# Kernel optimization log

Measured on AMD Instinct MI355X. Metric: run time of the kernel, lower is better.

## Reference

```python
import jax, jax.numpy as jnp
import numpy as np

N_PTILES = 4096
MAX_SOURCES = 1
PTILE_SLEN = 53  # odd -> slen == ptile_slen, size_lens is identity
N_BANDS = 1


def setup_inputs() -> dict:
    key = jax.random.key(0)
    k1, k2, k3, k4, k5, k6 = jax.random.split(key, 6)
    shape = (N_PTILES, MAX_SOURCES)
    gal = jax.random.uniform(k1, shape + (7,), dtype=jnp.float32)
    # realistic SIE lens params per _sample_lens_params: b in [5,30], q in (0,1)
    b = jax.random.uniform(k2, shape + (1,), dtype=jnp.float32) * 25.0 + 5.0
    centers = jax.random.normal(k3, shape + (2,), dtype=jnp.float32)
    q = jax.random.uniform(k4, shape + (1,), dtype=jnp.float32) * 0.8 + 0.1
    beta = (jax.random.uniform(k5, shape + (1,), dtype=jnp.float32) - 0.5) * (np.pi / 2)
    ellf = (1.0 - q) / (1.0 + q)
    e1 = ellf * jnp.cos(beta)
    e2 = ellf * jnp.sin(beta)
    lens_params = jnp.concatenate([gal, b, centers, e1, e2], axis=-1)  # [..., 12]
    bools = (jax.random.uniform(k6, shape + (1,), dtype=jnp.float32) < 0.7).astype(jnp.float32)
    return {"lens_params": lens_params, "lensed_galaxy_bools": bools}


def _render_unlensed(gal_p, slen):
    # Differentiable Gaussian stand-in for the (CPU galsim) unlensed source render.
    c = jnp.arange(slen, dtype=jnp.float32) - (slen - 1) / 2.0
    yy, xx = jnp.meshgrid(c, c, indexing="ij")
    flux = gal_p[:, 0] * 1000.0 + 100.0      # [N]
    sigma = gal_p[:, 3] * 3.0 + 1.0          # [N]
    r2 = xx[None] ** 2 + yy[None] ** 2       # [1, S, S]
    s2 = (sigma ** 2)[:, None, None]
    return flux[:, None, None] * jnp.exp(-0.5 * r2 / s2) / (2.0 * np.pi * s2)


def _sie_deflection(x, y, lens_p):
    # x, y: [1, S, S]; lens_p: [N, 5] -> (xg, yg): [N, S, S]
    b, cx, cy, e1, e2 = [lens_p[:, i][:, None, None] for i in range(5)]
    ell = jnp.sqrt(e1 ** 2 + e2 ** 2)
    q = (1.0 - ell) / (1.0 + ell)
    phirad = jnp.arctan(e2 / e1)
    cosp, sinp = jnp.cos(phirad), jnp.sin(phirad)
    xsie = (x - cx) * cosp + (y - cy) * sinp
    ysie = (y - cy) * cosp - (x - cx) * sinp
    r_ell = jnp.sqrt(q * xsie ** 2 + ysie ** 2 / q + 1e-12)
    qfact = jnp.sqrt(1.0 / q - q)
    eps = 0.001
    safe = jnp.maximum(qfact, eps)
    denom = r_ell + (r_ell == 0)
    xtg = jnp.where(qfact >= eps, b / safe * jnp.arctan(safe * xsie / denom), b * xsie / denom)
    ytg = jnp.where(qfact >= eps, b / safe * jnp.arctanh(safe * ysie / denom), b * ysie / denom)
    xg = xtg * cosp - ytg * sinp
    yg = ytg * cosp + xtg * sinp
    return xg, yg


def _bilinear(im, xs, ys):
    # im: [N, S, S]; xs (col coord), ys (row coord): [N, S, S]
    N, S, _ = im.shape
    x0 = jnp.clip(jnp.floor(xs).astype(jnp.int32), 0, S - 1)
    x1 = jnp.clip(jnp.floor(xs).astype(jnp.int32) + 1, 0, S - 1)
    y0 = jnp.clip(jnp.floor(ys).astype(jnp.int32), 0, S - 1)
    y1 = jnp.clip(jnp.floor(ys).astype(jnp.int32) + 1, 0, S - 1)
    flat = im.reshape(N, S * S)

    def g(yi, xi):
        return jnp.take_along_axis(flat, (yi * S + xi).reshape(N, -1), axis=1).reshape(N, S, S)

    x0f, x1f = x0.astype(im.dtype), x1.astype(im.dtype)
    y0f, y1f = y0.astype(im.dtype), y1.astype(im.dtype)
    # weights use the CLIPPED integer corners, matching bilinear_interpolate_numpy
    wa = (x1f - xs) * (y1f - ys)
    wb = (x1f - xs) * (ys - y0f)
    wc = (xs - x0f) * (y1f - ys)
    wd = (xs - x0f) * (ys - y0f)
    return g(y0, x0) * wa + g(y1, x0) * wb + g(y0, x1) * wc + g(y1, x1) * wd


def _forward(lens_params, lensed_galaxy_bools):
    n_ptiles, max_s, P = lens_params.shape
    z = lens_params.reshape(-1, P)
    gal_p, lens_p = z[:, :7], z[:, 7:]
    slen = PTILE_SLEN
    unlensed = _render_unlensed(gal_p, slen)            # [N, S, S]
    # grid exactly as lens_galsim: range [-nx//2, nx//2] over nx points
    nx = slen
    lo = float((-nx) // 2)   # -27 for nx=53
    hi = float(nx // 2)      # 26
    coords = (hi - lo) * jnp.arange(nx, dtype=jnp.float32) / (nx - 1) + lo
    x = jnp.broadcast_to(coords[None, :], (nx, nx))  # varies along columns
    y = jnp.broadcast_to(coords[:, None], (nx, nx))  # varies along rows
    xg, yg = _sie_deflection(x[None], y[None], lens_p)
    shift = float(nx // 2)
    lensed = _bilinear(unlensed, x[None] - xg + shift, y[None] - yg + shift)
    out = lensed.reshape(n_ptiles, max_s, N_BANDS, slen, slen)
    # render-all + mask is equivalent to the zeros-init + boolean-fill + final mask
    return out * lensed_galaxy_bools[..., None, None]


def reference(lens_params, lensed_galaxy_bools):
    return _forward(lens_params, lensed_galaxy_bools)
```

## Files before the change

kernel.cpp:

```cpp
#include <hip/hip_runtime.h>
#include <math.h>

#define SLEN 53
#define NPIX 2809
#define NPARAM 12
#define BLK 256
#define PW 16
#define NSLOT 11

__device__ __forceinline__ float fast_atan(float u) {
    float t = __builtin_fabsf(u);
    float rin = __builtin_amdgcn_rcpf(t);
    bool big = t > 1.0f;
    float w = big ? rin : t;
    bool mid = w > 0.4142135624f;
    float w2 = (w - 1.0f) * __builtin_amdgcn_rcpf(w + 1.0f);
    float x = mid ? w2 : w;
    float z = x * x;
    float p = ((8.05374449538e-2f * z - 1.38776856032e-1f) * z
               + 1.99777106478e-1f) * z - 3.33329491539e-1f;
    float r = __builtin_fmaf(p * z, x, x);
    r = mid ? r + 0.78539816339744831f : r;
    r = big ? 1.57079632679489662f - r : r;
    return __builtin_copysignf(r, u);
}

__device__ __forceinline__ float fast_atanh(float v) {
    float a = __builtin_fabsf(v);
    float t = (1.0f + a) * __builtin_amdgcn_rcpf(1.0f - a);
    float r = 0.34657359027997264f * __builtin_amdgcn_logf(t);
    return __builtin_copysignf(r, v);
}

__global__ __launch_bounds__(BLK) void prep_kernel(
    const float* __restrict__ lens_params,
    const float* __restrict__ bools,
    float* __restrict__ ws, int n_tiles)
{
    int t = blockIdx.x * blockDim.x + threadIdx.x;
    if (t >= n_tiles) return;
    const float* p = lens_params + t * NPARAM;
    const float bl   = bools[t];
    const float flux = p[0] * 1000.0f + 100.0f;
    const float sg   = p[3] * 3.0f + 1.0f;
    const float s2   = sg * sg;
    const float A    = bl * flux / (6.28318530717958647692f * s2);
    const float nh2  = -0.5f / s2 * 1.44269504088896340736f;
    const float b  = p[7], cx = p[8], cy = p[9], e1 = p[10], e2 = p[11];
    const float ell  = sqrtf(e1 * e1 + e2 * e2);
    const float q    = (1.0f - ell) / (1.0f + ell);
    const float qinv = 1.0f / q;
    const float ph   = atanf(e2 / e1);
    const float cosp = cosf(ph), sinp = sinf(ph);
    const float qf   = sqrtf(qinv - q);
    const float safe = fmaxf(qf, 0.001f);
    const float bos  = b / safe;
    float* w = ws + t * PW;
    w[0]  = bl;   w[1]  = A;    w[2]  = nh2;  w[3]  = cosp;
    w[4]  = sinp; w[5]  = q;    w[6]  = qinv; w[7]  = safe;
    w[8]  = bos;  w[9]  = cx;   w[10] = cy;   w[11] = b;
    w[12] = (qf >= 0.001f) ? 1.0f : 0.0f;
    w[13] = 0.0f; w[14] = 0.0f; w[15] = 0.0f;
}

template<bool MB>
__device__ __forceinline__ void run_tile(
    float* __restrict__ outp, int tid,
    const float* __restrict__ Ctab, const float* __restrict__ Etab,
    float A, float cosp, float sinp, float q, float qinv,
    float safe, float bos, float cx, float cy, float b)
{
    #pragma unroll
    for (int g = 0; g < 3; ++g) {
        const int nk = (g == 2) ? 3 : 4;
        float xc[4], yc[4], val[4];
        #pragma unroll
        for (int k = 0; k < 4; ++k) {
            if (k >= nk) break;
            const int slot = g * 4 + k;
            int idx = slot * BLK + tid;
            if (slot == NSLOT - 1) idx = min(idx, NPIX - 1);
            const unsigned i = ((unsigned)idx * 39569u) >> 21;
            const int j = idx - (int)i * 53;
            xc[k] = Ctab[j];
            yc[k] = Ctab[i];
        }
        #pragma unroll
        for (int k = 0; k < 4; ++k) {
            if (k >= nk) break;
            const float dx = xc[k] - cx, dy = yc[k] - cy;
            const float xsie = dx * cosp + dy * sinp;
            const float ysie = dy * cosp - dx * sinp;
            const float arg = __builtin_fmaf(q * xsie, xsie,
                              __builtin_fmaf(qinv * ysie, ysie, 1e-12f));
            const float rcp_r = __builtin_amdgcn_rsqf(arg);
            float xtg, ytg;
            if (MB) {
                xtg = bos * fast_atan(safe * xsie * rcp_r);
                ytg = bos * fast_atanh(safe * ysie * rcp_r);
            } else {
                xtg = b * xsie * rcp_r;
                ytg = b * ysie * rcp_r;
            }
            const float xg = xtg * cosp - ytg * sinp;
            const float yg = ytg * cosp + xtg * sinp;
            const float xs = (xc[k] - xg) + 26.0f;
            const float ys = (yc[k] - yg) + 26.0f;
            const float fx = __builtin_floorf(xs);
            const float fy = __builtin_floorf(ys);
            const float x0f = fminf(fmaxf(fx, 0.0f), 52.0f);
            const float x1f = fminf(fmaxf(fx + 1.0f, 0.0f), 52.0f);
            const float y0f = fminf(fmaxf(fy, 0.0f), 52.0f);
            const float y1f = fminf(fmaxf(fy + 1.0f, 0.0f), 52.0f);
            const int x0 = (int)x0f, x1 = (int)x1f;
            const int y0 = (int)y0f, y1 = (int)y1f;
            const float Fx = (x1f - xs) * Etab[x0] + (xs - x0f) * Etab[x1];
            const float Fy = (y1f - ys) * Etab[y0] + (ys - y0f) * Etab[y1];
            val[k] = A * Fx * Fy;
        }
        #pragma unroll
        for (int k = 0; k < 4; ++k) {
            if (k >= nk) break;
            const int slot = g * 4 + k;
            const int idx = slot * BLK + tid;
            if (slot < NSLOT - 1 || idx < NPIX) outp[idx] = val[k];
        }
    }
}

__global__ __launch_bounds__(BLK) void lgtd_kernel(
    const float* __restrict__ ws,
    float* __restrict__ out)
{
    const int tile = blockIdx.x;
    const float* w = ws + tile * PW;
    float* outp = out + (size_t)tile * NPIX;
    const int tid = threadIdx.x;

    const float bl = w[0];
    if (bl == 0.0f) {
        #pragma unroll
        for (int s = 0; s < NSLOT; ++s) {
            const int idx = s * BLK + tid;
            if (s < NSLOT - 1 || idx < NPIX) outp[idx] = 0.0f;
        }
        return;
    }

    const float A    = w[1],  nh2  = w[2],  cosp = w[3], sinp = w[4];
    const float q    = w[5],  qinv = w[6],  safe = w[7], bos  = w[8];
    const float cx   = w[9],  cy   = w[10], b    = w[11];
    const bool  mb   = (w[12] != 0.0f);

    __shared__ float Ctab[SLEN];
    __shared__ float Etab[SLEN];
    if (tid < SLEN) {
        const float kf = (float)tid;
        Ctab[tid] = 53.0f * kf / 52.0f - 27.0f;
        const float d = kf - 26.0f;
        Etab[tid] = __builtin_amdgcn_exp2f(nh2 * (d * d));
    }
    __syncthreads();

    if (mb)
        run_tile<true >(outp, tid, Ctab, Etab, A, cosp, sinp, q, qinv, safe, bos, cx, cy, b);
    else
        run_tile<false>(outp, tid, Ctab, Etab, A, cosp, sinp, q, qinv, safe, bos, cx, cy, b);
}

extern "C" void kernel_launch(void* const* d_in, const int* in_sizes, int n_in,
                              void* d_out, int out_size, void* d_ws, size_t ws_size,
                              hipStream_t stream) {
    const float* lens  = (const float*)d_in[0];
    const float* bools = (const float*)d_in[1];
    float* out = (float*)d_out;
    float* ws  = (float*)d_ws;
    const int n_tiles = in_sizes[1];
    prep_kernel<<<(n_tiles + BLK - 1) / BLK, BLK, 0, stream>>>(lens, bools, ws, n_tiles);
    lgtd_kernel<<<n_tiles, BLK, 0, stream>>>(ws, out);
}
```

Before: 88.38 us.

## Map wave lanes to columns and rows to waves; use minimax atan

New measurement: 87.94 us. About the same (-0.5%).

```diff
diff --git a/kernel.cpp b/kernel.cpp
--- a/kernel.cpp
+++ b/kernel.cpp
@@ -6,21 +6,20 @@
 #define NPARAM 12
 #define BLK 256
 #define PW 16
-#define NSLOT 11
 
 __device__ __forceinline__ float fast_atan(float u) {
     float t = __builtin_fabsf(u);
     float rin = __builtin_amdgcn_rcpf(t);
     bool big = t > 1.0f;
     float w = big ? rin : t;
-    bool mid = w > 0.4142135624f;
-    float w2 = (w - 1.0f) * __builtin_amdgcn_rcpf(w + 1.0f);
-    float x = mid ? w2 : w;
-    float z = x * x;
-    float p = ((8.05374449538e-2f * z - 1.38776856032e-1f) * z
-               + 1.99777106478e-1f) * z - 3.33329491539e-1f;
-    float r = __builtin_fmaf(p * z, x, x);
-    r = mid ? r + 0.78539816339744831f : r;
+    float z = w * w;
+    float p = -0.01172120f;
+    p = __builtin_fmaf(p, z,  0.05265332f);
+    p = __builtin_fmaf(p, z, -0.11643287f);
+    p = __builtin_fmaf(p, z,  0.19354346f);
+    p = __builtin_fmaf(p, z, -0.33262347f);
+    p = __builtin_fmaf(p, z,  0.99997726f);
+    float r = w * p;
     r = big ? 1.57079632679489662f - r : r;
     return __builtin_copysignf(r, u);
 }
@@ -65,66 +64,52 @@
 
 template<bool MB>
 __device__ __forceinline__ void run_tile(
-    float* __restrict__ outp, int tid,
-    const float* __restrict__ Ctab, const float* __restrict__ Etab,
+    float* __restrict__ outp, int lane, int wv, const float* __restrict__ Etab,
+    const float* __restrict__ Ctab,
     float A, float cosp, float sinp, float q, float qinv,
     float safe, float bos, float cx, float cy, float b)
 {
-    #pragma unroll
-    for (int g = 0; g < 3; ++g) {
-        const int nk = (g == 2) ? 3 : 4;
-        float xc[4], yc[4], val[4];
-        #pragma unroll
-        for (int k = 0; k < 4; ++k) {
-            if (k >= nk) break;
-            const int slot = g * 4 + k;
-            int idx = slot * BLK + tid;
-            if (slot == NSLOT - 1) idx = min(idx, NPIX - 1);
-            const unsigned i = ((unsigned)idx * 39569u) >> 21;
-            const int j = idx - (int)i * 53;
-            xc[k] = Ctab[j];
-            yc[k] = Ctab[i];
+    const float xcl  = Ctab[lane];
+    const float dx   = xcl - cx;
+    const float dxc  = dx * cosp;
+    const float dxs  = dx * sinp;
+    const float xc26 = xcl + 26.0f;
+
+    for (int r = wv; r < SLEN; r += 4) {
+        const float ycr  = Ctab[r];
+        const float dy   = ycr - cy;
+        const float t1   = dy * sinp;
+        const float t2   = dy * cosp;
+        const float yc26 = ycr + 26.0f;
+
+        const float xsie = dxc + t1;
+        const float ysie = t2 - dxs;
+        const float arg  = __builtin_fmaf(q * xsie, xsie,
+                           __builtin_fmaf(qinv * ysie, ysie, 1e-12f));
+        const float rcp_r = __builtin_amdgcn_rsqf(arg);
+        float xtg, ytg;
+        if (MB) {
+            xtg = bos * fast_atan(safe * xsie * rcp_r);
+            ytg = bos * fast_atanh(safe * ysie * rcp_r);
+        } else {
+            xtg = b * xsie * rcp_r;
+            ytg = b * ysie * rcp_r;
         }
-        #pragma unroll
-        for (int k = 0; k < 4; ++k) {
-            if (k >= nk) break;
-            const float dx = xc[k] - cx, dy = yc[k] - cy;
-            const float xsie = dx * cosp + dy * sinp;
-            const float ysie = dy * cosp - dx * sinp;
-            const float arg = __builtin_fmaf(q * xsie, xsie,
-                              __builtin_fmaf(qinv * ysie, ysie, 1e-12f));
-            const float rcp_r = __builtin_amdgcn_rsqf(arg);
-            float xtg, ytg;
-            if (MB) {
-                xtg = bos * fast_atan(safe * xsie * rcp_r);
-                ytg = bos * fast_atanh(safe * ysie * rcp_r);
-            } else {
-                xtg = b * xsie * rcp_r;
-                ytg = b * ysie * rcp_r;
-            }
-            const float xg = xtg * cosp - ytg * sinp;
-            const float yg = ytg * cosp + xtg * sinp;
-            const float xs = (xc[k] - xg) + 26.0f;
-            const float ys = (yc[k] - yg) + 26.0f;
-            const float fx = __builtin_floorf(xs);
-            const float fy = __builtin_floorf(ys);
-            const float x0f = fminf(fmaxf(fx, 0.0f), 52.0f);
-            const float x1f = fminf(fmaxf(fx + 1.0f, 0.0f), 52.0f);
-            const float y0f = fminf(fmaxf(fy, 0.0f), 52.0f);
-            const float y1f = fminf(fmaxf(fy + 1.0f, 0.0f), 52.0f);
-            const int x0 = (int)x0f, x1 = (int)x1f;
-            const int y0 = (int)y0f, y1 = (int)y1f;
-            const float Fx = (x1f - xs) * Etab[x0] + (xs - x0f) * Etab[x1];
-            const float Fy = (y1f - ys) * Etab[y0] + (ys - y0f) * Etab[y1];
-            val[k] = A * Fx * Fy;
-        }
-        #pragma unroll
-        for (int k = 0; k < 4; ++k) {
-            if (k >= nk) break;
-            const int slot = g * 4 + k;
-            const int idx = slot * BLK + tid;
-            if (slot < NSLOT - 1 || idx < NPIX) outp[idx] = val[k];
-        }
+        const float xg = xtg * cosp - ytg * sinp;
+        const float yg = ytg * cosp + xtg * sinp;
+        const float xs = xc26 - xg;
+        const float ys = yc26 - yg;
+        const float fx = __builtin_floorf(xs);
+        const float fy = __builtin_floorf(ys);
+        const float x0f = fminf(fmaxf(fx,        0.0f), 52.0f);
+        const float x1f = fminf(fmaxf(fx + 1.0f, 0.0f), 52.0f);
+        const float y0f = fminf(fmaxf(fy,        0.0f), 52.0f);
+        const float y1f = fminf(fmaxf(fy + 1.0f, 0.0f), 52.0f);
+        const int x0 = (int)x0f, x1 = (int)x1f;
+        const int y0 = (int)y0f, y1 = (int)y1f;
+        const float Fx = (x1f - xs) * Etab[x0] + (xs - x0f) * Etab[x1];
+        const float Fy = (y1f - ys) * Etab[y0] + (ys - y0f) * Etab[y1];
+        outp[r * SLEN + lane] = A * Fx * Fy;
     }
 }
 
@@ -140,9 +125,9 @@
     const float bl = w[0];
     if (bl == 0.0f) {
         #pragma unroll
-        for (int s = 0; s < NSLOT; ++s) {
+        for (int s = 0; s < 11; ++s) {
             const int idx = s * BLK + tid;
-            if (s < NSLOT - 1 || idx < NPIX) outp[idx] = 0.0f;
+            if (s < 10 || idx < NPIX) outp[idx] = 0.0f;
         }
         return;
     }
@@ -162,10 +147,14 @@
     }
     __syncthreads();
 
+    const int lane = tid & 63;
+    const int wv   = tid >> 6;
+    if (lane >= SLEN) return;
+
     if (mb)
-        run_tile<true >(outp, tid, Ctab, Etab, A, cosp, sinp, q, qinv, safe, bos, cx, cy, b);
+        run_tile<true >(outp, lane, wv, Etab, Ctab, A, cosp, sinp, q, qinv, safe, bos, cx, cy, b);
     else
-        run_tile<false>(outp, tid, Ctab, Etab, A, cosp, sinp, q, qinv, safe, bos, cx, cy, b);
+        run_tile<false>(outp, lane, wv, Etab, Ctab, A, cosp, sinp, q, qinv, safe, bos, cx, cy, b);
 }
 
 extern "C" void kernel_launch(void* const* d_in, const int* in_sizes, int n_in,
```
